# Optimization experiments

Hardware: AMD Instinct MI355X
Metric: run time of the kernel (lower is better)

## Reference

```python
import jax, jax.numpy as jnp
import numpy as np

B, L, H, W = 4, 5000, 256, 256
C_IN, DIM_LOI, N_PTS0, N_PTS1, DIM_FC, N_OUT_LINE = 256, 128, 32, 8, 1024, 2500
SCALE = N_PTS0 // N_PTS1  # MaxPool1d kernel/stride


def setup_inputs() -> dict:
    key = jax.random.key(0)
    ks = jax.random.split(key, 8)
    feature = jax.random.normal(ks[0], (B, C_IN, H, W), jnp.float32)
    # line endpoints in pixel coords of the 256x256 feature map
    lines = jax.random.uniform(ks[1], (B, L, 2, 2), jnp.float32) * (H - 1)
    s = lambda fan: 1.0 / np.sqrt(fan)
    fc1_w = (jax.random.normal(ks[2], (DIM_LOI, C_IN), jnp.float32) * s(C_IN))
    fc1_b = jnp.zeros((DIM_LOI,), jnp.float32)
    w1 = jax.random.normal(ks[3], (DIM_LOI * N_PTS1, DIM_FC), jnp.float32) * s(DIM_LOI * N_PTS1)
    b1 = jnp.zeros((DIM_FC,), jnp.float32)
    w2 = jax.random.normal(ks[4], (DIM_FC, DIM_FC), jnp.float32) * s(DIM_FC)
    b2 = jnp.zeros((DIM_FC,), jnp.float32)
    w3 = jax.random.normal(ks[5], (DIM_FC, 4), jnp.float32) * s(DIM_FC)
    b3 = jnp.zeros((4,), jnp.float32)
    return dict(feature=feature, lines=lines, fc1_w=fc1_w, fc1_b=fc1_b,
                w1=w1, b1=b1, w2=w2, b2=b2, w3=w3, b3=b3)


def reference(feature, lines, fc1_w, fc1_b, w1, b1, w2, b2, w3, b3):
    # fc1: 1x1 conv  [B,C_IN,H,W] -> [B,DIM_LOI,H,W]
    x = jnp.einsum('bchw,oc->bohw', feature, fc1_w) + fc1_b[None, :, None, None]

    # sample N_PTS0 points along each line (lerp between endpoints), minus 0.5
    lam = jnp.linspace(0.0, 1.0, N_PTS0, dtype=feature.dtype)[None, None, :, None]
    p = lines[:, :, 0:1, :] * lam + lines[:, :, 1:2, :] * (1.0 - lam) - 0.5  # [B,L,P,2]
    px, py = p[..., 0], p[..., 1]  # px indexes H (rows), py indexes W (cols)
    px0 = jnp.clip(jnp.floor(px), 0.0, H - 1.0)
    py0 = jnp.clip(jnp.floor(py), 0.0, W - 1.0)
    px1 = jnp.clip(px0 + 1.0, 0.0, H - 1.0)
    py1 = jnp.clip(py0 + 1.0, 0.0, W - 1.0)
    ix0, iy0 = px0.astype(jnp.int32), py0.astype(jnp.int32)
    ix1, iy1 = px1.astype(jnp.int32), py1.astype(jnp.int32)
    idx00 = ix0 * W + iy0
    idx10 = ix1 * W + iy0
    idx01 = ix0 * W + iy1
    idx11 = ix1 * W + iy1
    w00 = (px1 - px) * (py1 - py)
    w10 = (px - px0) * (py1 - py)
    w01 = (px1 - px) * (py - py0)
    w11 = (px - px0) * (py - py0)

    def gather_one(fmap, i00, i10, i01, i11, g00, g10, g01, g11):
        f = fmap.reshape(DIM_LOI, H * W)
        g = lambda idx: f[:, idx.reshape(-1)].reshape(DIM_LOI, L, N_PTS0)
        return g(i00) * g00 + g(i10) * g10 + g(i01) * g01 + g(i11) * g11

    xp = jax.vmap(gather_one)(x, idx00, idx10, idx01, idx11, w00, w10, w01, w11)
    # xp: [B, DIM_LOI, L, N_PTS0] -> maxpool along points -> [B, DIM_LOI, L, N_PTS1]
    xp = xp.reshape(B, DIM_LOI, L, N_PTS1, SCALE).max(-1)
    # reshape like torch: [N, DIM_LOI, N_PTS1] -> [N, DIM_LOI*N_PTS1] (channel-major)
    feat = xp.transpose(0, 2, 1, 3).reshape(B, L, DIM_LOI * N_PTS1)

    # fc2 MLP -> 4 logits
    h = jax.nn.relu(feat @ w1 + b1)
    h = jax.nn.relu(h @ w2 + b2)
    logits = h @ w3 + b3  # [B, L, 4]
    s = jax.nn.softmax(logits, axis=-1)

    # threshold conditions
    keep = ((s[..., 1] > 0.25) | (s[..., 2] > 0.25) | (s[..., 3] > 0.25)) & (s[..., 0] < 0.25)

    def select(p0, s0, m):
        cnt = m.sum()
        key = jnp.where(m, jnp.argmax(s0, -1), -1)  # masked-out get -1 -> sorted last
        order = jnp.argsort(-key)  # stable desc sort of argmax class
        idx = order[jnp.arange(N_OUT_LINE) % jnp.maximum(cnt, 1)]
        lo = jnp.where(cnt > 0, p0[idx], 0.0)
        so = jnp.where(cnt > 0, s0[idx], 0.0)
        return lo, so

    lines_out, score_out = jax.vmap(select)(lines, s, keep)
    return lines_out, score_out, s
```

## Files before the change

### kernel.cpp

```cpp
#include <hip/hip_runtime.h>
#include <cstdint>
#include <cstddef>

#define B_     4
#define L_     5000
#define H_     256
#define W_     256
#define HW_    65536
#define CIN_   256
#define DLOI_  128
#define NPTS0_ 32
#define NPTS1_ 8
#define DFC_   1024
#define NOUT_  2500
#define M_     (B_*L_)
#define MPAD_  20096
#define NBAND_ 157

typedef _Float16 f16;
typedef _Float16 f16x4 __attribute__((ext_vector_type(4)));
typedef _Float16 f16x8 __attribute__((ext_vector_type(8)));
typedef float    f32x4 __attribute__((ext_vector_type(4)));

__device__ __forceinline__ void gload16(const void* g, void* l) {
  __builtin_amdgcn_global_load_lds(
      (const __attribute__((address_space(1))) void*)g,
      (__attribute__((address_space(3))) void*)l, 16, 0, 0);
}

__global__ __launch_bounds__(256) void k_wsplit(const float* __restrict__ src,
                                                f16* __restrict__ h,
                                                f16* __restrict__ l) {
  int i = (blockIdx.x * 256 + threadIdx.x) * 4;
  float4 v = *(const float4*)(src + i);
  f16 h0 = (f16)v.x, h1 = (f16)v.y, h2 = (f16)v.z, h3 = (f16)v.w;
  *(f16x4*)(h + i) = (f16x4){h0, h1, h2, h3};
  *(f16x4*)(l + i) = (f16x4){(f16)(v.x - (float)h0), (f16)(v.y - (float)h1),
                             (f16)(v.z - (float)h2), (f16)(v.w - (float)h3)};
}

__global__ __launch_bounds__(256) void k_conv_mfma(const float* __restrict__ fin,
                                                   const f16* __restrict__ wh,
                                                   const f16* __restrict__ wl,
                                                   const float* __restrict__ bias,
                                                   float* __restrict__ xout) {
  __shared__ f16 lds[16384];
  const int t = threadIdx.x;
  const int P0 = blockIdx.x * 128;
  const int b  = P0 >> 16;
  const int ph0 = P0 & 65535;
  const int lane = t & 63, wave = t >> 6;
  const int quad = lane >> 4, lo = lane & 15;
  const int wm = wave >> 1, wn = wave & 1;

  const int c_base = (t & 7) * 4;
  const int p = (t >> 3) * 4;
  const size_t fbase = (size_t)b * CIN_ * HW_ + (size_t)ph0 + p;

  const int srow = t >> 2;
  const int skb  = (t & 3) * 16;
  const char* gBh = (const char*)wh + (size_t)srow * 512 + skb;
  const char* gBl = (const char*)wl + (size_t)srow * 512 + skb;
  char* ldsB = (char*)lds + t * 16;

  f32x4 acc[4][4];
  #pragma unroll
  for (int mt = 0; mt < 4; mt++)
    #pragma unroll
    for (int nt = 0; nt < 4; nt++) acc[mt][nt] = (f32x4){0.f, 0.f, 0.f, 0.f};

  float4 av[4], nv[4];
  #pragma unroll
  for (int j = 0; j < 4; j++)
    av[j] = *(const float4*)(fin + fbase + (size_t)(c_base + j) * HW_);

  for (int kc = 0; kc < 8; kc++) {
    const size_t bko = (size_t)kc * 64;
    gload16(gBh + bko,         ldsB + 16384);
    gload16(gBh + 32768 + bko, ldsB + 16384 + 4096);
    gload16(gBl + bko,         ldsB + 24576);
    gload16(gBl + 32768 + bko, ldsB + 24576 + 4096);

    #pragma unroll
    for (int i = 0; i < 4; i++) {
      f16 hh[4], ll[4];
      #pragma unroll
      for (int j = 0; j < 4; j++) {
        float v = ((const float*)&av[j])[i];
        hh[j] = (f16)v;
        ll[j] = (f16)(v - (float)hh[j]);
      }
      *(f16x4*)(&lds[(p + i) * 32 + c_base])        = (f16x4){hh[0], hh[1], hh[2], hh[3]};
      *(f16x4*)(&lds[4096 + (p + i) * 32 + c_base]) = (f16x4){ll[0], ll[1], ll[2], ll[3]};
    }
    __syncthreads();

    if (kc < 7) {
      #pragma unroll
      for (int j = 0; j < 4; j++)
        nv[j] = *(const float4*)(fin + fbase + (size_t)((kc + 1) * 32 + c_base + j) * HW_);
    }

    f16x8 ah[4], al[4], bh4[4], bl4[4];
    #pragma unroll
    for (int mt = 0; mt < 4; mt++) {
      int row = wm * 64 + mt * 16 + lo;
      ah[mt] = *(const f16x8*)(&lds[row * 32 + quad * 8]);
      al[mt] = *(const f16x8*)(&lds[4096 + row * 32 + quad * 8]);
    }
    #pragma unroll
    for (int nt = 0; nt < 4; nt++) {
      int row = wn * 64 + nt * 16 + lo;
      bh4[nt] = *(const f16x8*)(&lds[8192 + row * 32 + quad * 8]);
      bl4[nt] = *(const f16x8*)(&lds[12288 + row * 32 + quad * 8]);
    }
    #pragma unroll
    for (int mt = 0; mt < 4; mt++)
      #pragma unroll
      for (int nt = 0; nt < 4; nt++) {
        acc[mt][nt] = __builtin_amdgcn_mfma_f32_16x16x32_f16(ah[mt], bh4[nt], acc[mt][nt], 0, 0, 0);
        acc[mt][nt] = __builtin_amdgcn_mfma_f32_16x16x32_f16(ah[mt], bl4[nt], acc[mt][nt], 0, 0, 0);
        acc[mt][nt] = __builtin_amdgcn_mfma_f32_16x16x32_f16(al[mt], bh4[nt], acc[mt][nt], 0, 0, 0);
      }
    __syncthreads();
    #pragma unroll
    for (int j = 0; j < 4; j++) av[j] = nv[j];
  }

  #pragma unroll
  for (int nt = 0; nt < 4; nt++) {
    int col = wn * 64 + nt * 16 + lo;
    float bv = bias[col];
    #pragma unroll
    for (int mt = 0; mt < 4; mt++) {
      int rowb = P0 + wm * 64 + mt * 16 + quad * 4;
      #pragma unroll
      for (int r = 0; r < 4; r++)
        xout[(size_t)(rowb + r) * DLOI_ + col] = acc[mt][nt][r] + bv;
    }
  }
}

__global__ __launch_bounds__(128) void k_sample(const float* __restrict__ x,
                                                const float* __restrict__ lines,
                                                f16* __restrict__ fh,
                                                f16* __restrict__ fl) {
  const int blk = blockIdx.x;
  const int b = blk / L_;
  const int c = threadIdx.x;
  const float* ln = lines + (size_t)blk * 4;
  const float e0x = ln[0], e0y = ln[1], e1x = ln[2], e1y = ln[3];
  const float* xb = x + (size_t)b * HW_ * DLOI_;
  f16x8 vh, vl;
  for (int q = 0; q < NPTS1_; q++) {
    float m = -1e30f;
    #pragma unroll
    for (int r = 0; r < 4; r++) {
      int i = q * 4 + r;
      float lam = (float)i * (1.0f / 31.0f);
      float px = e0x * lam + e1x * (1.f - lam) - 0.5f;
      float py = e0y * lam + e1y * (1.f - lam) - 0.5f;
      float px0 = fminf(fmaxf(floorf(px), 0.f), 255.f);
      float py0 = fminf(fmaxf(floorf(py), 0.f), 255.f);
      float px1 = fminf(px0 + 1.f, 255.f);
      float py1 = fminf(py0 + 1.f, 255.f);
      int ix0 = (int)px0, iy0 = (int)py0, ix1 = (int)px1, iy1 = (int)py1;
      float w00 = (px1 - px) * (py1 - py);
      float w10 = (px - px0) * (py1 - py);
      float w01 = (px1 - px) * (py - py0);
      float w11 = (px - px0) * (py - py0);
      float v = w00 * xb[(size_t)(ix0 * W_ + iy0) * DLOI_ + c]
              + w10 * xb[(size_t)(ix1 * W_ + iy0) * DLOI_ + c]
              + w01 * xb[(size_t)(ix0 * W_ + iy1) * DLOI_ + c]
              + w11 * xb[(size_t)(ix1 * W_ + iy1) * DLOI_ + c];
      m = fmaxf(m, v);
    }
    f16 h = (f16)m;
    vh[q] = h;
    vl[q] = (f16)(m - (float)h);
  }
  *(f16x8*)(fh + (size_t)blk * DFC_ + c * 8) = vh;
  *(f16x8*)(fl + (size_t)blk * DFC_ + c * 8) = vl;
}

__global__ __launch_bounds__(256) void k_tsplit(const float* __restrict__ Wsrc,
                                                f16* __restrict__ Th,
                                                f16* __restrict__ Tl) {
  __shared__ float tile[32][33];
  const int bj = blockIdx.x, bi = blockIdx.y;
  const int tx = threadIdx.x & 31, ty = threadIdx.x >> 5;
  #pragma unroll
  for (int r = ty; r < 32; r += 8)
    tile[r][tx] = Wsrc[(size_t)(bi * 32 + r) * 1024 + bj * 32 + tx];
  __syncthreads();
  #pragma unroll
  for (int r = ty; r < 32; r += 8) {
    float v = tile[tx][r];
    f16 h = (f16)v;
    size_t o = (size_t)(bj * 32 + r) * 1024 + bi * 32 + tx;
    Th[o] = h;
    Tl[o] = (f16)(v - (float)h);
  }
}

#define BKT_    32
#define NTT_    (DFC_/BKT_)
#define SLOT_B_ 49152
#define AH_O_   0
#define AL_O_   8192
#define BH_O_   16384
#define BL_O_   32768

template <bool SPLIT_OUT>
__global__ __launch_bounds__(512, 2) void k_gemm_f16x3(
    const f16* __restrict__ Ah, const f16* __restrict__ Al,
    const f16* __restrict__ Bh, const f16* __restrict__ Bl,
    const float* __restrict__ bias,
    f16* __restrict__ Oh, f16* __restrict__ Ol,
    const float* __restrict__ w3, float* __restrict__ part) {
  __shared__ f16 lds[3 * SLOT_B_ / 2];
  char* ldsc = (char*)lds;

  const int orig = blockIdx.x;
  const int xcd = orig & 7, bidx = orig >> 3;
  const int qq = 628 >> 3, rr = 628 & 7;
  const int wg = (xcd < rr ? xcd * (qq + 1) : rr * (qq + 1) + (xcd - rr) * qq) + bidx;
  const int band = wg >> 2;
  const int nb   = wg & 3;
  const int r0 = band * 128;
  const int n0 = nb * 256;

  const int t = threadIdx.x;
  const int lane = t & 63, wave = t >> 6;
  const int quad = lane >> 4, lo = lane & 15;
  const int wm = wave >> 2, wn = wave & 3;

  const uint32_t usA  = (uint32_t)t ^ (((uint32_t)t >> 3) & 7);
  const uint32_t uB1  = (uint32_t)t + 512u;
  const uint32_t usB1 = uB1 ^ ((uB1 >> 3) & 7);
  const size_t sA  = (size_t)(usA  >> 2) * 2048 + (size_t)(usA  & 3) * 16;
  const size_t sB1 = (size_t)(usB1 >> 2) * 2048 + (size_t)(usB1 & 3) * 16;

  const char* gAh  = (const char*)Ah + (size_t)r0 * 2048 + sA;
  const char* gAl  = (const char*)Al + (size_t)r0 * 2048 + sA;
  const char* gBh0 = (const char*)Bh + (size_t)n0 * 2048 + sA;
  const char* gBh1 = (const char*)Bh + (size_t)n0 * 2048 + sB1;
  const char* gBl0 = (const char*)Bl + (size_t)n0 * 2048 + sA;
  const char* gBl1 = (const char*)Bl + (size_t)n0 * 2048 + sB1;

  const int dAh  = AH_O_ + t * 16;
  const int dAl  = AL_O_ + t * 16;
  const int dBh0 = BH_O_ + t * 16;
  const int dBh1 = BH_O_ + 8192 + t * 16;
  const int dBl0 = BL_O_ + t * 16;
  const int dBl1 = BL_O_ + 8192 + t * 16;

  int roffA[4], roffB[4];
  #pragma unroll
  for (int mt = 0; mt < 4; mt++) {
    int r = wm * 64 + mt * 16 + lo;
    roffA[mt] = (((r * 4 + quad) ^ ((r >> 1) & 7)) << 4);
  }
  #pragma unroll
  for (int nt = 0; nt < 4; nt++) {
    int r = wn * 64 + nt * 16 + lo;
    roffB[nt] = (((r * 4 + quad) ^ ((r >> 1) & 7)) << 4);
  }

  f32x4 acc[4][4];
  #pragma unroll
  for (int mt = 0; mt < 4; mt++)
    #pragma unroll
    for (int nt = 0; nt < 4; nt++) acc[mt][nt] = (f32x4){0.f, 0.f, 0.f, 0.f};

  gload16(gAh,        ldsc + dAh);
  gload16(gAl,        ldsc + dAl);
  gload16(gBh0,       ldsc + dBh0);
  gload16(gBh1,       ldsc + dBh1);
  gload16(gBl0,       ldsc + dBl0);
  gload16(gBl1,       ldsc + dBl1);
  gload16(gAh  + 64,  ldsc + SLOT_B_ + dAh);
  gload16(gAl  + 64,  ldsc + SLOT_B_ + dAl);
  gload16(gBh0 + 64,  ldsc + SLOT_B_ + dBh0);
  gload16(gBh1 + 64,  ldsc + SLOT_B_ + dBh1);
  gload16(gBl0 + 64,  ldsc + SLOT_B_ + dBl0);
  gload16(gBl1 + 64,  ldsc + SLOT_B_ + dBl1);
  asm volatile("s_waitcnt vmcnt(6)" ::: "memory");
  __builtin_amdgcn_s_barrier();

  int cur = 0, stg = 2;
  for (int tt = 0; tt < NTT_; ++tt) {
    const char* sc = ldsc + cur * SLOT_B_;
    char* sw = ldsc + stg * SLOT_B_;
    const size_t go = (size_t)tt * 64 + 128;
    const bool pf = (tt + 2 < NTT_);

    f16x8 ah[4], al[4], bh[4], bl[4];

    #pragma unroll
    for (int mt = 0; mt < 4; mt++)
      ah[mt] = *(const f16x8*)(sc + AH_O_ + roffA[mt]);
    #pragma unroll
    for (int nt = 0; nt < 4; nt++)
      bh[nt] = *(const f16x8*)(sc + BH_O_ + roffB[nt]);
    if (pf) { gload16(gAh + go, sw + dAh); gload16(gAl + go, sw + dAl); }
    __builtin_amdgcn_s_barrier();
    asm volatile("s_waitcnt lgkmcnt(0)" ::: "memory");
    __builtin_amdgcn_sched_barrier(0);
    __builtin_amdgcn_s_setprio(1);
    #pragma unroll
    for (int mt = 0; mt < 4; mt++)
      #pragma unroll
      for (int nt = 0; nt < 4; nt++)
        acc[mt][nt] = __builtin_amdgcn_mfma_f32_16x16x32_f16(ah[mt], bh[nt], acc[mt][nt], 0, 0, 0);
    __builtin_amdgcn_s_setprio(0);
    __builtin_amdgcn_s_barrier();

    #pragma unroll
    for (int mt = 0; mt < 4; mt++)
      al[mt] = *(const f16x8*)(sc + AL_O_ + roffA[mt]);
    if (pf) { gload16(gBh0 + go, sw + dBh0); gload16(gBh1 + go, sw + dBh1); }
    __builtin_amdgcn_s_barrier();
    asm volatile("s_waitcnt lgkmcnt(0)" ::: "memory");
    __builtin_amdgcn_sched_barrier(0);
    __builtin_amdgcn_s_setprio(1);
    #pragma unroll
    for (int mt = 0; mt < 4; mt++)
      #pragma unroll
      for (int nt = 0; nt < 4; nt++)
        acc[mt][nt] = __builtin_amdgcn_mfma_f32_16x16x32_f16(al[mt], bh[nt], acc[mt][nt], 0, 0, 0);
    __builtin_amdgcn_s_setprio(0);
    __builtin_amdgcn_s_barrier();

    #pragma unroll
    for (int nt = 0; nt < 4; nt++)
      bl[nt] = *(const f16x8*)(sc + BL_O_ + roffB[nt]);
    if (pf) { gload16(gBl0 + go, sw + dBl0); gload16(gBl1 + go, sw + dBl1); }
    __builtin_amdgcn_s_barrier();
    asm volatile("s_waitcnt lgkmcnt(0)" ::: "memory");
    __builtin_amdgcn_sched_barrier(0);
    __builtin_amdgcn_s_setprio(1);
    #pragma unroll
    for (int mt = 0; mt < 4; mt++)
      #pragma unroll
      for (int nt = 0; nt < 4; nt++)
        acc[mt][nt] = __builtin_amdgcn_mfma_f32_16x16x32_f16(ah[mt], bl[nt], acc[mt][nt], 0, 0, 0);
    __builtin_amdgcn_s_setprio(0);
    if (tt < NTT_ - 2) asm volatile("s_waitcnt vmcnt(6)" ::: "memory");
    else               asm volatile("s_waitcnt vmcnt(0)" ::: "memory");
    __builtin_amdgcn_s_barrier();

    cur = (cur == 2) ? 0 : cur + 1;
    stg = (stg == 2) ? 0 : stg + 1;
  }

  if (SPLIT_OUT) {
    #pragma unroll
    for (int nt = 0; nt < 4; nt++) {
      const int col = n0 + wn * 64 + nt * 16 + lo;
      const float bv = bias[col];
      #pragma unroll
      for (int mt = 0; mt < 4; mt++) {
        const int rowb = r0 + wm * 64 + mt * 16 + quad * 4;
        #pragma unroll
        for (int r = 0; r < 4; r++) {
          const int row = rowb + r;
          if (row < M_) {
            float v = fmaxf(acc[mt][nt][r] + bv, 0.f);
            f16 h = (f16)v;
            Oh[(size_t)row * DFC_ + col] = h;
            Ol[(size_t)row * DFC_ + col] = (f16)(v - (float)h);
          }
        }
      }
    }
  } else {
    const int slot = nb * 4 + wn;
    #pragma unroll
    for (int mt = 0; mt < 4; mt++) {
      float p[4][4];
      #pragma unroll
      for (int r = 0; r < 4; r++)
        #pragma unroll
        for (int j = 0; j < 4; j++) p[r][j] = 0.f;
      #pragma unroll
      for (int nt = 0; nt < 4; nt++) {
        const int col = n0 + wn * 64 + nt * 16 + lo;
        const float bv = bias[col];
        float4 wv = *(const float4*)(w3 + col * 4);
        #pragma unroll
        for (int r = 0; r < 4; r++) {
          float v = fmaxf(acc[mt][nt][r] + bv, 0.f);
          p[r][0] = fmaf(v, wv.x, p[r][0]);
          p[r][1] = fmaf(v, wv.y, p[r][1]);
          p[r][2] = fmaf(v, wv.z, p[r][2]);
          p[r][3] = fmaf(v, wv.w, p[r][3]);
        }
      }
      #pragma unroll
      for (int r = 0; r < 4; r++)
        #pragma unroll
        for (int j = 0; j < 4; j++) {
          p[r][j] += __shfl_xor(p[r][j], 1);
          p[r][j] += __shfl_xor(p[r][j], 2);
          p[r][j] += __shfl_xor(p[r][j], 4);
          p[r][j] += __shfl_xor(p[r][j], 8);
        }
      if (lo == 0) {
        const int rowb = r0 + wm * 64 + mt * 16 + quad * 4;
        #pragma unroll
        for (int r = 0; r < 4; r++)
          *(float4*)(part + ((size_t)slot * MPAD_ + rowb + r) * 4) =
              make_float4(p[r][0], p[r][1], p[r][2], p[r][3]);
      }
    }
  }
}

__global__ __launch_bounds__(256) void k_head2(const float* __restrict__ part,
                                               const float* __restrict__ b3,
                                               float* __restrict__ s_out,
                                               int* __restrict__ key_out) {
  const int row = blockIdx.x * 256 + threadIdx.x;
  if (row >= M_) return;
  float l0 = b3[0], l1 = b3[1], l2 = b3[2], l3 = b3[3];
  #pragma unroll
  for (int sl = 0; sl < 16; sl++) {
    float4 p = *(const float4*)(part + ((size_t)sl * MPAD_ + row) * 4);
    l0 += p.x; l1 += p.y; l2 += p.z; l3 += p.w;
  }
  float mx = fmaxf(fmaxf(l0, l1), fmaxf(l2, l3));
  float e0 = expf(l0 - mx), e1 = expf(l1 - mx), e2 = expf(l2 - mx), e3 = expf(l3 - mx);
  float inv = 1.f / (e0 + e1 + e2 + e3);
  float s0 = e0 * inv, s1 = e1 * inv, s2 = e2 * inv, s3 = e3 * inv;
  *(float4*)(s_out + (size_t)row * 4) = make_float4(s0, s1, s2, s3);
  bool keep = ((s1 > 0.25f) || (s2 > 0.25f) || (s3 > 0.25f)) && (s0 < 0.25f);
  int am = 0; float best = s0;
  if (s1 > best) { best = s1; am = 1; }
  if (s2 > best) { best = s2; am = 2; }
  if (s3 > best) { best = s3; am = 3; }
  key_out[row] = keep ? am : -1;
}

__global__ __launch_bounds__(1024) void k_select(const int* __restrict__ key,
                                                 const float* __restrict__ lines,
                                                 const float* __restrict__ s,
                                                 float* __restrict__ out_lines,
                                                 float* __restrict__ out_score) {
  __shared__ int s_ord[L_];
  __shared__ int s_scan[1024];
  __shared__ int s_tot[5];
  const int b = blockIdx.x;
  const int t = threadIdx.x;
  const int base_l = t * 5;
  int cls[5];
  int c[5] = {0, 0, 0, 0, 0};
  #pragma unroll
  for (int i = 0; i < 5; i++) {
    int l = base_l + i;
    int cl = -1;
    if (l < L_) {
      int k = key[b * L_ + l];
      cl = (k < 0) ? 4 : (3 - k);
      c[cl]++;
    }
    cls[i] = cl;
  }
  int pf[5];
  for (int cc = 0; cc < 5; cc++) {
    s_scan[t] = c[cc];
    __syncthreads();
    for (int off = 1; off < 1024; off <<= 1) {
      int add = (t >= off) ? s_scan[t - off] : 0;
      __syncthreads();
      s_scan[t] += add;
      __syncthreads();
    }
    pf[cc] = s_scan[t] - c[cc];
    if (t == 1023) s_tot[cc] = s_scan[1023];
    __syncthreads();
  }
  int basec[5];
  basec[0] = 0;
  #pragma unroll
  for (int cc = 1; cc < 5; cc++) basec[cc] = basec[cc - 1] + s_tot[cc - 1];
  int run[5] = {0, 0, 0, 0, 0};
  #pragma unroll
  for (int i = 0; i < 5; i++) {
    if (cls[i] >= 0) {
      int cl = cls[i];
      int pos = basec[cl] + pf[cl] + run[cl];
      run[cl]++;
      s_ord[pos] = base_l + i;
    }
  }
  const int cnt = L_ - s_tot[4];
  __syncthreads();
  for (int j = t; j < NOUT_; j += 1024) {
    float4 lv = make_float4(0.f, 0.f, 0.f, 0.f);
    float4 sv = make_float4(0.f, 0.f, 0.f, 0.f);
    if (cnt > 0) {
      int idx = s_ord[j % cnt];
      lv = *(const float4*)(lines + (size_t)(b * L_ + idx) * 4);
      sv = *(const float4*)(s + (size_t)(b * L_ + idx) * 4);
    }
    *(float4*)(out_lines + (size_t)(b * NOUT_ + j) * 4) = lv;
    *(float4*)(out_score + (size_t)(b * NOUT_ + j) * 4) = sv;
  }
}

extern "C" void kernel_launch(void* const* d_in, const int* in_sizes, int n_in,
                              void* d_out, int out_size, void* d_ws, size_t ws_size,
                              hipStream_t stream) {
  const float* feature = (const float*)d_in[0];
  const float* lines   = (const float*)d_in[1];
  const float* fc1_w   = (const float*)d_in[2];
  const float* fc1_b   = (const float*)d_in[3];
  const float* w1      = (const float*)d_in[4];
  const float* b1      = (const float*)d_in[5];
  const float* w2      = (const float*)d_in[6];
  const float* b2      = (const float*)d_in[7];
  const float* w3      = (const float*)d_in[8];
  const float* b3      = (const float*)d_in[9];

  float* out_lines = (float*)d_out;
  float* out_score = out_lines + B_ * NOUT_ * 4;
  float* s_out     = out_score + B_ * NOUT_ * 4;

  char* ws = (char*)d_ws;
  float* x    = (float*)(ws);
  f16*   h1h  = (f16*)(ws);
  f16*   h1l  = (f16*)(ws + 41156608ull);
  float* part = (float*)(ws + 82313216ull);
  f16*   fh   = (f16*)(ws + 134217728ull);
  f16*   fl   = (f16*)(ws + 134217728ull + 41156608ull);
  f16*   wt1h = (f16*)(ws + 216530944ull);
  f16*   wt1l = (f16*)(ws + 216530944ull + 2097152ull);
  f16*   wt2h = (f16*)(ws + 216530944ull + 2ull * 2097152ull);
  f16*   wt2l = (f16*)(ws + 216530944ull + 3ull * 2097152ull);
  int*   keys = (int*)(ws + 224919552ull);
  f16*   wc_h = (f16*)(ws + 224999552ull);
  f16*   wc_l = (f16*)(ws + 224999552ull + 65536ull);

  k_wsplit<<<dim3(32), 256, 0, stream>>>(fc1_w, wc_h, wc_l);
  k_tsplit<<<dim3(32, 32), 256, 0, stream>>>(w1, wt1h, wt1l);
  k_tsplit<<<dim3(32, 32), 256, 0, stream>>>(w2, wt2h, wt2l);
  k_conv_mfma<<<dim3((B_ * HW_) / 128), 256, 0, stream>>>(feature, wc_h, wc_l, fc1_b, x);
  k_sample<<<dim3(M_), 128, 0, stream>>>(x, lines, fh, fl);
  k_gemm_f16x3<true><<<dim3(628), 512, 0, stream>>>(
      fh, fl, wt1h, wt1l, b1, h1h, h1l, nullptr, nullptr);
  k_gemm_f16x3<false><<<dim3(628), 512, 0, stream>>>(
      h1h, h1l, wt2h, wt2l, b2, nullptr, nullptr, w3, part);
  k_head2<<<dim3((M_ + 255) / 256), 256, 0, stream>>>(part, b3, s_out, keys);
  k_select<<<dim3(B_), 1024, 0, stream>>>(keys, lines, s_out, out_lines, out_score);
}
```

Baseline: 895.8 us.

## Merge GEMM k-step phases into one barrier and stage epilogue stores through LDS

The three per-iteration sub-phases, each with its own barrier and lgkmcnt wait, are collapsed into one. All six global-to-LDS prefetches are issued up front, all A/B hi/lo fragments are read together, and the three MFMA groups run back to back. The split-output epilogue now writes hi/lo fp16 results into a per-wave swizzled LDS tile and then emits coalesced 16-byte global stores, replacing scattered 2-byte stores. This aims to cut synchronization stalls and uncoalesced writes, at the cost of more live registers. There is also some risk that reusing LDS for the epilogue, and changing the final vmcnt waits, is unsafe if prefetches or other waves are still active.

```diff
diff --git a/kernel.cpp b/kernel.cpp
--- a/kernel.cpp
+++ b/kernel.cpp
@@ -295,59 +295,49 @@
     const size_t go = (size_t)tt * 64 + 128;
     const bool pf = (tt + 2 < NTT_);
 
-    f16x8 ah[4], al[4], bh[4], bl[4];
-
+    if (pf) {
+      gload16(gAh  + go, sw + dAh);
+      gload16(gAl  + go, sw + dAl);
+      gload16(gBh0 + go, sw + dBh0);
+      gload16(gBh1 + go, sw + dBh1);
+      gload16(gBl0 + go, sw + dBl0);
+      gload16(gBl1 + go, sw + dBl1);
+    }
+
+    f16x8 ah[4], bh[4], al[4], bl[4];
     #pragma unroll
     for (int mt = 0; mt < 4; mt++)
       ah[mt] = *(const f16x8*)(sc + AH_O_ + roffA[mt]);
     #pragma unroll
     for (int nt = 0; nt < 4; nt++)
       bh[nt] = *(const f16x8*)(sc + BH_O_ + roffB[nt]);
-    if (pf) { gload16(gAh + go, sw + dAh); gload16(gAl + go, sw + dAl); }
-    __builtin_amdgcn_s_barrier();
-    asm volatile("s_waitcnt lgkmcnt(0)" ::: "memory");
-    __builtin_amdgcn_sched_barrier(0);
+    #pragma unroll
+    for (int mt = 0; mt < 4; mt++)
+      al[mt] = *(const f16x8*)(sc + AL_O_ + roffA[mt]);
+    #pragma unroll
+    for (int nt = 0; nt < 4; nt++)
+      bl[nt] = *(const f16x8*)(sc + BL_O_ + roffB[nt]);
+
     __builtin_amdgcn_s_setprio(1);
     #pragma unroll
     for (int mt = 0; mt < 4; mt++)
       #pragma unroll
       for (int nt = 0; nt < 4; nt++)
         acc[mt][nt] = __builtin_amdgcn_mfma_f32_16x16x32_f16(ah[mt], bh[nt], acc[mt][nt], 0, 0, 0);
-    __builtin_amdgcn_s_setprio(0);
-    __builtin_amdgcn_s_barrier();
-
-    #pragma unroll
-    for (int mt = 0; mt < 4; mt++)
-      al[mt] = *(const f16x8*)(sc + AL_O_ + roffA[mt]);
-    if (pf) { gload16(gBh0 + go, sw + dBh0); gload16(gBh1 + go, sw + dBh1); }
-    __builtin_amdgcn_s_barrier();
-    asm volatile("s_waitcnt lgkmcnt(0)" ::: "memory");
-    __builtin_amdgcn_sched_barrier(0);
-    __builtin_amdgcn_s_setprio(1);
     #pragma unroll
     for (int mt = 0; mt < 4; mt++)
       #pragma unroll
       for (int nt = 0; nt < 4; nt++)
         acc[mt][nt] = __builtin_amdgcn_mfma_f32_16x16x32_f16(al[mt], bh[nt], acc[mt][nt], 0, 0, 0);
-    __builtin_amdgcn_s_setprio(0);
-    __builtin_amdgcn_s_barrier();
-
-    #pragma unroll
-    for (int nt = 0; nt < 4; nt++)
-      bl[nt] = *(const f16x8*)(sc + BL_O_ + roffB[nt]);
-    if (pf) { gload16(gBl0 + go, sw + dBl0); gload16(gBl1 + go, sw + dBl1); }
-    __builtin_amdgcn_s_barrier();
-    asm volatile("s_waitcnt lgkmcnt(0)" ::: "memory");
-    __builtin_amdgcn_sched_barrier(0);
-    __builtin_amdgcn_s_setprio(1);
     #pragma unroll
     for (int mt = 0; mt < 4; mt++)
       #pragma unroll
       for (int nt = 0; nt < 4; nt++)
         acc[mt][nt] = __builtin_amdgcn_mfma_f32_16x16x32_f16(ah[mt], bl[nt], acc[mt][nt], 0, 0, 0);
     __builtin_amdgcn_s_setprio(0);
-    if (tt < NTT_ - 2) asm volatile("s_waitcnt vmcnt(6)" ::: "memory");
-    else               asm volatile("s_waitcnt vmcnt(0)" ::: "memory");
+
+    if (tt < NTT_ - 2)       asm volatile("s_waitcnt vmcnt(6)" ::: "memory");
+    else if (tt == NTT_ - 2) asm volatile("s_waitcnt vmcnt(0)" ::: "memory");
     __builtin_amdgcn_s_barrier();
 
     cur = (cur == 2) ? 0 : cur + 1;
@@ -355,23 +345,40 @@
   }
 
   if (SPLIT_OUT) {
-    #pragma unroll
-    for (int nt = 0; nt < 4; nt++) {
-      const int col = n0 + wn * 64 + nt * 16 + lo;
-      const float bv = bias[col];
-      #pragma unroll
-      for (int mt = 0; mt < 4; mt++) {
-        const int rowb = r0 + wm * 64 + mt * 16 + quad * 4;
+    char* ep = ldsc + wave * 16384;
+    #pragma unroll
+    for (int mt = 0; mt < 4; mt++)
+      #pragma unroll
+      for (int nt = 0; nt < 4; nt++) {
+        const int col = n0 + wn * 64 + nt * 16 + lo;
+        const float bv = bias[col];
+        const int col_l = nt * 16 + lo;
         #pragma unroll
         for (int r = 0; r < 4; r++) {
-          const int row = rowb + r;
-          if (row < M_) {
-            float v = fmaxf(acc[mt][nt][r] + bv, 0.f);
-            f16 h = (f16)v;
-            Oh[(size_t)row * DFC_ + col] = h;
-            Ol[(size_t)row * DFC_ + col] = (f16)(v - (float)h);
-          }
+          const int rl = mt * 16 + quad * 4 + r;
+          float v = fmaxf(acc[mt][nt][r] + bv, 0.f);
+          f16 h = (f16)v;
+          f16 lw = (f16)(v - (float)h);
+          const int byte = rl * 128 + ((((col_l >> 3) ^ (rl & 7)) << 4)) + (col_l & 7) * 2;
+          *(f16*)(ep + byte) = h;
+          *(f16*)(ep + 8192 + byte) = lw;
         }
+      }
+    asm volatile("s_waitcnt lgkmcnt(0)" ::: "memory");
+    __builtin_amdgcn_sched_barrier(0);
+    const int r8 = lane >> 3;
+    const int ck = lane & 7;
+    #pragma unroll
+    for (int g = 0; g < 8; g++) {
+      const int rl = g * 8 + r8;
+      const int grow = r0 + wm * 64 + rl;
+      const int swz = ((ck ^ (rl & 7)) << 4);
+      f16x8 vh = *(const f16x8*)(ep + rl * 128 + swz);
+      f16x8 vl = *(const f16x8*)(ep + 8192 + rl * 128 + swz);
+      if (grow < M_) {
+        const size_t gb = (size_t)grow * 2048 + (size_t)(n0 + wn * 64) * 2 + ck * 16;
+        *(f16x8*)((char*)Oh + gb) = vh;
+        *(f16x8*)((char*)Ol + gb) = vl;
       }
     }
   } else {
```

New measurement: 872.7 us. 2.6% less time.
